# Optimization experiments

Measured on AMD Instinct MI355X. Metric: run time of the kernel, lower is better.

Reference implementation:

```python
import jax, jax.numpy as jnp
import numpy as np
from jax import lax

EMBED = 512
HEADS = 8
KD = EMBED // HEADS  # key_dim == head_dim (value_factor=1)


def setup_inputs() -> dict:
    key = jax.random.key(0)
    ks = jax.random.split(key, 13)
    b, h, w = 4, 128, 128
    s = 0.02
    return {
        "x": jax.random.normal(ks[0], (b, h, w, EMBED), jnp.float32),
        "mask_h": jax.random.normal(ks[1], (HEADS, h, h), jnp.float32),
        "mask_w": jax.random.normal(ks[2], (HEADS, w, w), jnp.float32),
        "Wq": jax.random.normal(ks[3], (EMBED, EMBED), jnp.float32) * s,
        "bq": jnp.zeros((EMBED,), jnp.float32),
        "Wk": jax.random.normal(ks[4], (EMBED, EMBED), jnp.float32) * s,
        "bk": jnp.zeros((EMBED,), jnp.float32),
        "Wv": jax.random.normal(ks[5], (EMBED, EMBED), jnp.float32) * s,
        "bv": jnp.zeros((EMBED,), jnp.float32),
        "lepe_w": jax.random.normal(ks[6], (5, 5, 1, EMBED), jnp.float32) * s,  # depthwise 5x5, HWIO
        "lepe_b": jnp.zeros((EMBED,), jnp.float32),
        "Wo": jax.random.normal(ks[7], (EMBED, EMBED), jnp.float32) * s,
        "bo": jnp.zeros((EMBED,), jnp.float32),
    }


def reference(x, mask_h, mask_w, Wq, bq, Wk, bk, Wv, bv, lepe_w, lepe_b, Wo, bo):
    b, h, w, _ = x.shape
    scaling = KD ** -0.5
    q = x @ Wq + bq                      # (b,h,w,C)
    k = (x @ Wk + bk) * scaling
    v = x @ Wv + bv

    # depthwise-conv positional term (LePE), 5x5 pad 2, groups=C
    lepe = lax.conv_general_dilated(
        v, lepe_w, window_strides=(1, 1), padding=[(2, 2), (2, 2)],
        dimension_numbers=("NHWC", "HWIO", "NHWC"), feature_group_count=EMBED,
    ) + lepe_b

    qr = q.reshape(b, h, w, HEADS, KD)
    kr = k.reshape(b, h, w, HEADS, KD)
    vr = v.reshape(b, h, w, HEADS, KD)

    # width-axis attention (per row), additive per-head decay mask
    sw = jnp.einsum("bhqnd,bhknd->bhnqk", qr, kr) + mask_w[None, None]  # (b,h,n,w,w)
    Aw = jax.nn.softmax(sw, axis=-1)
    o1 = jnp.einsum("bhnqk,bhknd->bhqnd", Aw, vr)                       # (b,h,w,n,d)

    # height-axis attention (per column) on the width-pass output
    sh = jnp.einsum("bqwnd,bkwnd->bwnqk", qr, kr) + mask_h[None, None]  # (b,w,n,h,h)
    Ah = jax.nn.softmax(sh, axis=-1)
    o2 = jnp.einsum("bwnqk,bkwnd->bqwnd", Ah, o1)                       # (b,h,w,n,d)

    out = o2.reshape(b, h, w, EMBED) + lepe
    return out @ Wo + bo
```

## Files before the change

kernel.cpp:

```cpp
#include <hip/hip_runtime.h>
#include <stdint.h>
#include <stddef.h>

typedef unsigned short u16;
typedef __attribute__((ext_vector_type(8))) short bf16x8;
typedef __attribute__((ext_vector_type(4))) short bf16x4;
typedef __attribute__((ext_vector_type(4))) float f32x4;

__device__ __forceinline__ u16 f2bf(float f) {
  union { float f; uint32_t u; } v; v.f = f;
  uint32_t u = v.u;
  return (u16)((u + 0x7FFFu + ((u >> 16) & 1u)) >> 16);
}
__device__ __forceinline__ float bf2f(u16 b) {
  union { uint32_t u; float f; } v; v.u = ((uint32_t)b) << 16;
  return v.f;
}

__device__ __forceinline__ void glds16(const u16* g, u16* l) {
  __builtin_amdgcn_global_load_lds((const __attribute__((address_space(1))) void*)g,
                                   (__attribute__((address_space(3))) void*)l, 16, 0, 0);
}

__device__ __forceinline__ uint32_t lds_addr(const u16* p) {
  return (uint32_t)(uintptr_t)(const __attribute__((address_space(3))) u16*)p;
}

#define MFMA(a, b, c) __builtin_amdgcn_mfma_f32_16x16x32_bf16((a), (b), (c), 0, 0, 0)


__global__ __launch_bounds__(256) void k_cvt_bf16(const float* __restrict__ in,
                                                  u16* __restrict__ out, int n) {
  int i = (blockIdx.x * 256 + threadIdx.x) * 8;
  if (i >= n) return;
  const float4* p = (const float4*)(in + i);
  float4 a = p[0], b = p[1];
  union { bf16x8 v; u16 s[8]; } o;
  o.s[0] = f2bf(a.x); o.s[1] = f2bf(a.y); o.s[2] = f2bf(a.z); o.s[3] = f2bf(a.w);
  o.s[4] = f2bf(b.x); o.s[5] = f2bf(b.y); o.s[6] = f2bf(b.z); o.s[7] = f2bf(b.w);
  *(bf16x8*)(out + i) = o.v;
}


__global__ __launch_bounds__(256) void k_build_w(
    const float* __restrict__ Wq, const float* __restrict__ Wk,
    const float* __restrict__ Wv, const float* __restrict__ Wo,
    const float* __restrict__ bq, const float* __restrict__ bk,
    const float* __restrict__ bv,
    u16* __restrict__ wqkvT, u16* __restrict__ woT, float* __restrict__ bias)
{
  __shared__ u16 tl[64 * 73];
  const int bid = blockIdx.x;
  const int mtx = bid >> 6;
  const int tr = (bid >> 3) & 7, tc = bid & 7;
  const float* W = (mtx == 0) ? Wq : (mtx == 1) ? Wk : (mtx == 2) ? Wv : Wo;
  const float s = (mtx == 1) ? 0.125f : 1.0f;
  const int t = threadIdx.x;
  const int lr = t >> 6, lc = t & 63;
  #pragma unroll
  for (int it = 0; it < 16; ++it) {
    int k = tr * 64 + it * 4 + lr;
    int n = tc * 64 + lc;
    tl[lc * 73 + it * 4 + lr] = f2bf(W[(size_t)k * 512 + n] * s);
  }
  __syncthreads();
  u16* dst = (mtx == 3) ? woT : (wqkvT + (size_t)mtx * 512 * 512);
  #pragma unroll
  for (int it = 0; it < 16; ++it) {
    int n = tc * 64 + it * 4 + lr;
    int k = tr * 64 + lc;
    dst[(size_t)n * 512 + k] = tl[(it * 4 + lr) * 73 + lc];
  }
  if (bid < 6) {
    int i = bid * 256 + t;
    const float* B = (i < 512) ? bq : (i < 1024) ? bk : bv;
    float sc = (i >= 512 && i < 1024) ? 0.125f : 1.0f;
    bias[i] = B[i & 511] * sc;
  }
}


__device__ __forceinline__ void stageH(const u16* __restrict__ src, int ld, size_t grow0,
                                       int kt, int row0, u16* lmat, int t) {
  #pragma unroll
  for (int it = 0; it < 2; ++it) {
    int e = it * 4096 + t * 8;
    int row = row0 + (e >> 6);
    int ch = (e >> 3) & 7;
    int cs = ch ^ (row & 7);
    glds16(src + (grow0 + row) * (size_t)ld + kt * 64 + cs * 8, lmat + row * 64 + ch * 8);
  }
}

__device__ __forceinline__ bf16x8 ldfrag(const u16* lmat, int row, int c) {
  return *(const bf16x8*)(lmat + row * 64 + ((c ^ (row & 7)) << 3));
}

template<bool STAGE, bool VM8>
__device__ __forceinline__ void process_tile(
    const u16* __restrict__ A, int lda, size_t rowA0,
    const u16* __restrict__ BT, int ldb, size_t rowB0,
    u16* LAc, u16* LBc, int nxt,
    int wm, int wn, int fq, int fr, int t,
    f32x4 (&acc)[2][4][2][2])
{
  bf16x8 bA[4][2], bB[2][2][2];
  #pragma unroll
  for (int n = 0; n < 2; ++n)
    #pragma unroll
    for (int kk = 0; kk < 2; ++kk)
      bB[0][n][kk] = ldfrag(LBc, wn * 32 + n * 16 + fr, kk * 4 + fq);
  #pragma unroll
  for (int m = 0; m < 4; ++m)
    #pragma unroll
    for (int kk = 0; kk < 2; ++kk)
      bA[m][kk] = ldfrag(LAc, wm * 64 + m * 16 + fr, kk * 4 + fq);
  __builtin_amdgcn_s_setprio(1);
  #pragma unroll
  for (int m = 0; m < 4; ++m)
    #pragma unroll
    for (int n = 0; n < 2; ++n)
      #pragma unroll
      for (int kk = 0; kk < 2; ++kk)
        acc[0][m][0][n] = MFMA(bA[m][kk], bB[0][n][kk], acc[0][m][0][n]);
  __builtin_amdgcn_s_setprio(0);
  __builtin_amdgcn_s_barrier();
  #pragma unroll
  for (int n = 0; n < 2; ++n)
    #pragma unroll
    for (int kk = 0; kk < 2; ++kk)
      bB[1][n][kk] = ldfrag(LBc, 128 + wn * 32 + n * 16 + fr, kk * 4 + fq);
  if (STAGE) {
    stageH(A, lda, rowA0, nxt, 0, LAc, t);
    stageH(BT, ldb, rowB0, nxt, 0, LBc, t);
  }
  __builtin_amdgcn_s_setprio(1);
  #pragma unroll
  for (int m = 0; m < 4; ++m)
    #pragma unroll
    for (int n = 0; n < 2; ++n)
      #pragma unroll
      for (int kk = 0; kk < 2; ++kk)
        acc[0][m][1][n] = MFMA(bA[m][kk], bB[1][n][kk], acc[0][m][1][n]);
  __builtin_amdgcn_s_setprio(0);
  __builtin_amdgcn_s_barrier();
  #pragma unroll
  for (int m = 0; m < 4; ++m)
    #pragma unroll
    for (int kk = 0; kk < 2; ++kk)
      bA[m][kk] = ldfrag(LAc, 128 + wm * 64 + m * 16 + fr, kk * 4 + fq);
  if (STAGE) stageH(BT, ldb, rowB0, nxt, 128, LBc, t);
  __builtin_amdgcn_s_setprio(1);
  #pragma unroll
  for (int m = 0; m < 4; ++m)
    #pragma unroll
    for (int n = 0; n < 2; ++n)
      #pragma unroll
      for (int kk = 0; kk < 2; ++kk)
        acc[1][m][0][n] = MFMA(bA[m][kk], bB[0][n][kk], acc[1][m][0][n]);
  __builtin_amdgcn_s_setprio(0);
  __builtin_amdgcn_s_barrier();
  if (STAGE) stageH(A, lda, rowA0, nxt, 128, LAc, t);
  __builtin_amdgcn_s_setprio(1);
  #pragma unroll
  for (int m = 0; m < 4; ++m)
    #pragma unroll
    for (int n = 0; n < 2; ++n)
      #pragma unroll
      for (int kk = 0; kk < 2; ++kk)
        acc[1][m][1][n] = MFMA(bA[m][kk], bB[1][n][kk], acc[1][m][1][n]);
  __builtin_amdgcn_s_setprio(0);
  if (VM8) asm volatile("s_waitcnt vmcnt(8)" ::: "memory");
  else     asm volatile("s_waitcnt vmcnt(0)" ::: "memory");
  __builtin_amdgcn_s_barrier();
}

template<bool OUT_F32, int NTN>
__global__ __launch_bounds__(512, 2) void k_gemm256(
    const u16* __restrict__ A, int lda,
    const u16* __restrict__ BT, int ldb,
    const float* __restrict__ bias,
    void* __restrict__ Cp, int ldc)
{
  __shared__ u16 lds[65536];
  u16* LA0 = lds;
  u16* LB0 = lds + 16384;
  u16* LA1 = lds + 32768;
  u16* LB1 = lds + 49152;

  const int t = threadIdx.x, l = t & 63, w = t >> 6;
  const int wm = w >> 2, wn = w & 3;
  const int fq = l >> 4, fr = l & 15;

  const int bid = blockIdx.x;
  const int cpx = gridDim.x >> 3;
  const int swz = (bid & 7) * cpx + (bid >> 3);
  const int tn = swz % NTN, tm = swz / NTN;
  const size_t rowA0 = (size_t)tm * 256;
  const size_t rowB0 = (size_t)tn * 256;

  f32x4 acc[2][4][2][2];
  #pragma unroll
  for (int a = 0; a < 2; ++a)
    #pragma unroll
    for (int m = 0; m < 4; ++m)
      #pragma unroll
      for (int b = 0; b < 2; ++b)
        #pragma unroll
        for (int n = 0; n < 2; ++n) acc[a][m][b][n] = (f32x4){0.f, 0.f, 0.f, 0.f};

  stageH(A,  lda, rowA0, 0, 0,   LA0, t); stageH(A,  lda, rowA0, 0, 128, LA0, t);
  stageH(BT, ldb, rowB0, 0, 0,   LB0, t); stageH(BT, ldb, rowB0, 0, 128, LB0, t);
  stageH(A,  lda, rowA0, 1, 0,   LA1, t); stageH(A,  lda, rowA0, 1, 128, LA1, t);
  stageH(BT, ldb, rowB0, 1, 0,   LB1, t); stageH(BT, ldb, rowB0, 1, 128, LB1, t);
  asm volatile("s_waitcnt vmcnt(8)" ::: "memory");
  __builtin_amdgcn_s_barrier();

  for (int i = 0; i < 3; ++i) {
    process_tile<true, true>(A, lda, rowA0, BT, ldb, rowB0, LA0, LB0, 2 * i + 2,
                             wm, wn, fq, fr, t, acc);
    process_tile<true, true>(A, lda, rowA0, BT, ldb, rowB0, LA1, LB1, 2 * i + 3,
                             wm, wn, fq, fr, t, acc);
  }
  process_tile<false, false>(A, lda, rowA0, BT, ldb, rowB0, LA0, LB0, 0,
                             wm, wn, fq, fr, t, acc);
  process_tile<false, false>(A, lda, rowA0, BT, ldb, rowB0, LA1, LB1, 0,
                             wm, wn, fq, fr, t, acc);

  #pragma unroll
  for (int nh = 0; nh < 2; ++nh)
    #pragma unroll
    for (int n = 0; n < 2; ++n) {
      int col = (int)rowB0 + nh * 128 + wn * 32 + n * 16 + fr;
      float bb = bias[col];
      #pragma unroll
      for (int mh = 0; mh < 2; ++mh)
        #pragma unroll
        for (int m = 0; m < 4; ++m) {
          #pragma unroll
          for (int r = 0; r < 4; ++r) {
            size_t row = rowA0 + mh * 128 + wm * 64 + m * 16 + fq * 4 + r;
            float v = acc[mh][m][nh][n][r] + bb;
            if (OUT_F32) ((float*)Cp)[row * ldc + col] = v;
            else         ((u16*)Cp)[row * ldc + col] = f2bf(v);
          }
        }
    }
}


__global__ __launch_bounds__(256) void k_lepe(
    const u16* __restrict__ qkv, const float* __restrict__ w5,
    const float* __restrict__ lb, u16* __restrict__ outp)
{
  __shared__ u16 wlds[12800];
  #pragma unroll
  for (int j = 0; j < 50; ++j) {
    int idx = j * 256 + threadIdx.x;
    wlds[idx] = f2bf(w5[idx]);
  }
  __syncthreads();

  const int t = threadIdx.x, w = t >> 6, l = t & 63;
  const int c0 = l << 3;
  const int bid = blockIdx.x;
  const int x = (bid & 31) * 4 + w;
  const int y0 = ((bid >> 5) & 15) * 8;
  const int b = bid >> 9;

  float acc[8][8];
  {
    float4 b0 = *(const float4*)(lb + c0);
    float4 b1 = *(const float4*)(lb + c0 + 4);
    #pragma unroll
    for (int tt = 0; tt < 8; ++tt) {
      acc[tt][0] = b0.x; acc[tt][1] = b0.y; acc[tt][2] = b0.z; acc[tt][3] = b0.w;
      acc[tt][4] = b1.x; acc[tt][5] = b1.y; acc[tt][6] = b1.z; acc[tt][7] = b1.w;
    }
  }

  #pragma unroll
  for (int dx = 0; dx < 5; ++dx) {
    int xx = x + dx - 2;
    if ((unsigned)xx < 128u) {
      float wreg[5][8];
      #pragma unroll
      for (int dy = 0; dy < 5; ++dy) {
        union { bf16x8 v; u16 s[8]; } w8;
        w8.v = *(const bf16x8*)(wlds + (dy * 5 + dx) * 512 + c0);
        #pragma unroll
        for (int j = 0; j < 8; ++j) wreg[dy][j] = bf2f(w8.s[j]);
      }
      #pragma unroll
      for (int r = 0; r < 12; ++r) {
        int yy = y0 + r - 2;
        if ((unsigned)yy < 128u) {
          union { bf16x8 v; u16 s[8]; } v8;
          v8.v = *(const bf16x8*)(qkv + (size_t)((b * 128 + yy) * 128 + xx) * 1536
                                  + 1024 + c0);
          float vf[8];
          #pragma unroll
          for (int j = 0; j < 8; ++j) vf[j] = bf2f(v8.s[j]);
          #pragma unroll
          for (int tt = 0; tt < 8; ++tt) {
            int dy = r - tt;
            if (dy >= 0 && dy <= 4) {
              #pragma unroll
              for (int j = 0; j < 8; ++j)
                acc[tt][j] += vf[j] * wreg[dy][j];
            }
          }
        }
      }
    }
  }

  #pragma unroll
  for (int tt = 0; tt < 8; ++tt) {
    size_t tok = (size_t)(b * 128 + y0 + tt) * 128 + x;
    union { bf16x8 v; u16 s[8]; } ov;
    #pragma unroll
    for (int j = 0; j < 8; ++j) ov.s[j] = f2bf(acc[tt][j]);
    *(bf16x8*)(outp + tok * 512 + c0) = ov.v;
  }
}


template<int AXIS>
__global__ __launch_bounds__(512) void k_attn(
    const u16* qkv, const float* __restrict__ mask,
    const u16* __restrict__ lepe, u16* outp)
{
  __shared__ u16 smem[24576];
  u16* q_s = smem;
  u16* k_s = smem + 8192;
  u16* vL  = smem + 16384;
  u16* P   = smem;

  const int t = threadIdx.x, w = t >> 6, l = t & 63;
  const int fq = l >> 4, fr = l & 15;
  const int line = blockIdx.x, head = blockIdx.y, b = blockIdx.z;
  const int coff = head * 64;
  const size_t base0 = (AXIS == 0) ? ((size_t)(b * 128 + line) * 128)
                                   : ((size_t)b * 16384 + line);
  const size_t tstr = (AXIS == 0) ? 1 : 128;

  #pragma unroll
  for (int it = 0; it < 2; ++it) {
    int ee = it * 4096 + t * 8;
    int row = ee >> 6;
    int cs = ((ee >> 3) & 7) ^ (row & 7);
    size_t tok = base0 + (size_t)row * tstr;
    glds16(qkv + tok * 1536 +       coff + cs * 8, q_s + it * 4096 + w * 512);
    glds16(qkv + tok * 1536 + 512 + coff + cs * 8, k_s + it * 4096 + w * 512);
  }
  #pragma unroll
  for (int p = 0; p < 2; ++p) {
    int c = p * 512 + t;
    int kt = (c >> 5) * 4 + ((c >> 1) & 3);
    int d0 = ((c >> 3) & 3) * 16 + (c & 1) * 8;
    size_t tok = base0 + (size_t)kt * tstr;
    glds16(qkv + tok * 1536 + 1024 + coff + d0, vL + c * 8);
  }
  __syncthreads();

  f32x4 acc[8];
  #pragma unroll
  for (int n = 0; n < 8; ++n) acc[n] = (f32x4){0.f, 0.f, 0.f, 0.f};

  #pragma unroll
  for (int kk = 0; kk < 2; ++kk) {
    int arow = w * 16 + fr;
    int ac = (kk * 4 + fq) ^ (arow & 7);
    bf16x8 af = *(const bf16x8*)(q_s + arow * 64 + ac * 8);
    #pragma unroll
    for (int n = 0; n < 8; ++n) {
      int brow = n * 16 + fr;
      int bc = (kk * 4 + fq) ^ (brow & 7);
      bf16x8 bfr = *(const bf16x8*)(k_s + brow * 64 + bc * 8);
      acc[n] = MFMA(af, bfr, acc[n]);
    }
  }

  const float* mbase = mask + (size_t)head * 16384;
  const int q0 = w * 16 + fq * 4;
  #pragma unroll
  for (int n = 0; n < 8; ++n) {
    const float* mp = mbase + (size_t)q0 * 128 + n * 16 + fr;
    #pragma unroll
    for (int r = 0; r < 4; ++r) acc[n][r] += mp[(size_t)r * 128];
  }
  #pragma unroll
  for (int r = 0; r < 4; ++r) {
    float mx = acc[0][r];
    #pragma unroll
    for (int n = 1; n < 8; ++n) mx = fmaxf(mx, acc[n][r]);
    mx = fmaxf(mx, __shfl_xor(mx, 1));
    mx = fmaxf(mx, __shfl_xor(mx, 2));
    mx = fmaxf(mx, __shfl_xor(mx, 4));
    mx = fmaxf(mx, __shfl_xor(mx, 8));
    float sum = 0.f;
    #pragma unroll
    for (int n = 0; n < 8; ++n) {
      float ev = __expf(acc[n][r] - mx);
      acc[n][r] = ev; sum += ev;
    }
    sum += __shfl_xor(sum, 1);
    sum += __shfl_xor(sum, 2);
    sum += __shfl_xor(sum, 4);
    sum += __shfl_xor(sum, 8);
    float inv = 1.0f / sum;
    #pragma unroll
    for (int n = 0; n < 8; ++n) acc[n][r] *= inv;
  }
  __syncthreads();

  #pragma unroll
  for (int r = 0; r < 4; ++r) {
    int row = q0 + r;
    int swz = (row & 7) << 4;
    #pragma unroll
    for (int n = 0; n < 8; ++n) {
      int col = n * 16 + fr;
      *(u16*)((char*)P + row * 256 + ((2 * col) ^ swz)) = f2bf(acc[n][r]);
    }
  }
  __syncthreads();

  f32x4 o[4];
  #pragma unroll
  for (int n = 0; n < 4; ++n) o[n] = (f32x4){0.f, 0.f, 0.f, 0.f};

  const uint32_t vbase = lds_addr(vL) + (uint32_t)(fq * 1024 + fr * 8);
  #pragma unroll
  for (int kt = 0; kt < 4; ++kt) {
    int arow = w * 16 + fr;
    bf16x8 af = *(const bf16x8*)((const char*)P + arow * 256 +
                 (((kt * 4 + fq) << 4) ^ ((arow & 7) << 4)));
    bf16x4 lo0, hi0, lo1, hi1, lo2, hi2, lo3, hi3;
    {
      uint32_t a0 = vbase + kt * 4096;
      uint32_t a1 = a0 + 128;
      uint32_t a2 = a0 + 256;
      uint32_t a3 = a0 + 384;
      asm volatile("ds_read_b64_tr_b16 %0, %1" : "=v"(lo0) : "v"(a0));
      asm volatile("ds_read_b64_tr_b16 %0, %1 offset:512" : "=v"(hi0) : "v"(a0));
      asm volatile("ds_read_b64_tr_b16 %0, %1" : "=v"(lo1) : "v"(a1));
      asm volatile("ds_read_b64_tr_b16 %0, %1 offset:512" : "=v"(hi1) : "v"(a1));
      asm volatile("ds_read_b64_tr_b16 %0, %1" : "=v"(lo2) : "v"(a2));
      asm volatile("ds_read_b64_tr_b16 %0, %1 offset:512" : "=v"(hi2) : "v"(a2));
      asm volatile("ds_read_b64_tr_b16 %0, %1" : "=v"(lo3) : "v"(a3));
      asm volatile("ds_read_b64_tr_b16 %0, %1 offset:512" : "=v"(hi3) : "v"(a3));
    }
    asm volatile("s_waitcnt lgkmcnt(0)" ::: "memory");
    __builtin_amdgcn_sched_barrier(0);
    union { bf16x4 h[2]; bf16x8 v; } u0, u1, u2, u3;
    u0.h[0] = lo0; u0.h[1] = hi0;
    u1.h[0] = lo1; u1.h[1] = hi1;
    u2.h[0] = lo2; u2.h[1] = hi2;
    u3.h[0] = lo3; u3.h[1] = hi3;
    o[0] = MFMA(af, u0.v, o[0]);
    o[1] = MFMA(af, u1.v, o[1]);
    o[2] = MFMA(af, u2.v, o[2]);
    o[3] = MFMA(af, u3.v, o[3]);
  }

  #pragma unroll
  for (int r = 0; r < 4; ++r) {
    int i = q0 + r;
    size_t tok = base0 + (size_t)i * tstr;
    #pragma unroll
    for (int n = 0; n < 4; ++n) {
      int d = n * 16 + fr;
      float v = o[n][r];
      if (AXIS == 1) {
        v += bf2f(lepe[tok * 512 + coff + d]);
        outp[tok * 1536 + coff + d] = f2bf(v);
      } else {
        outp[tok * 1536 + 1024 + coff + d] = f2bf(v);
      }
    }
  }
}


extern "C" void kernel_launch(void* const* d_in, const int* in_sizes, int n_in,
                              void* d_out, int out_size, void* d_ws, size_t ws_size,
                              hipStream_t stream) {
  const float* x  = (const float*)d_in[0];
  const float* mh = (const float*)d_in[1];
  const float* mw = (const float*)d_in[2];
  const float* Wq = (const float*)d_in[3];
  const float* bq = (const float*)d_in[4];
  const float* Wk = (const float*)d_in[5];
  const float* bk = (const float*)d_in[6];
  const float* Wv = (const float*)d_in[7];
  const float* bv = (const float*)d_in[8];
  const float* w5 = (const float*)d_in[9];
  const float* lb = (const float*)d_in[10];
  const float* Wo = (const float*)d_in[11];
  const float* bo = (const float*)d_in[12];

  char* ws = (char*)d_ws;
  u16*   qkv   = (u16*)ws;
  u16*   wqkvT = (u16*)(ws + 201326592);
  u16*   woT   = (u16*)(ws + 202899456);
  float* bqkv  = (float*)(ws + 203423744);

  char* od = (char*)d_out;
  u16* xb   = (u16*)od;
  u16* lepe = (u16*)(od + 67108864);

  k_cvt_bf16<<<16384, 256, 0, stream>>>(x, xb, 33554432);
  k_build_w<<<256, 256, 0, stream>>>(Wq, Wk, Wv, Wo, bq, bk, bv, wqkvT, woT, bqkv);

  k_gemm256<false, 6><<<1536, 512, 0, stream>>>(xb, 512, wqkvT, 512, bqkv,
                                                qkv, 1536);

  k_lepe<<<2048, 256, 0, stream>>>(qkv, w5, lb, lepe);

  k_attn<0><<<dim3(128, 8, 4), 512, 0, stream>>>(qkv, mw, nullptr, qkv);
  k_attn<1><<<dim3(128, 8, 4), 512, 0, stream>>>(qkv, mh, lepe, qkv);

  k_gemm256<true, 2><<<512, 512, 0, stream>>>(qkv, 1536, woT, 512, bo, d_out, 512);
}
```

Before: 416.1 us.

## Fuse fp32-to-bf16 conversion of x into the QKV GEMM A-tile staging

Removes the standalone x conversion kernel and has a new QKV GEMM load fp32 A tiles through registers, converting them to bf16 before writing to LDS. B tiles still use direct global-to-LDS loads. This drops a full write and re-read of the bf16 copy of x (about 64MB of traffic) and one launch. In exchange, each of the six column tiles rereads fp32 A, doubling A read bytes, and the register staging adds VGPR pressure and latency in the pipelined loop.

```diff
diff --git a/kernel.cpp b/kernel.cpp
--- a/kernel.cpp
+++ b/kernel.cpp
@@ -27,19 +27,6 @@
 }
 
 #define MFMA(a, b, c) __builtin_amdgcn_mfma_f32_16x16x32_bf16((a), (b), (c), 0, 0, 0)
-
-
-__global__ __launch_bounds__(256) void k_cvt_bf16(const float* __restrict__ in,
-                                                  u16* __restrict__ out, int n) {
-  int i = (blockIdx.x * 256 + threadIdx.x) * 8;
-  if (i >= n) return;
-  const float4* p = (const float4*)(in + i);
-  float4 a = p[0], b = p[1];
-  union { bf16x8 v; u16 s[8]; } o;
-  o.s[0] = f2bf(a.x); o.s[1] = f2bf(a.y); o.s[2] = f2bf(a.z); o.s[3] = f2bf(a.w);
-  o.s[4] = f2bf(b.x); o.s[5] = f2bf(b.y); o.s[6] = f2bf(b.z); o.s[7] = f2bf(b.w);
-  *(bf16x8*)(out + i) = o.v;
-}
 
 
 __global__ __launch_bounds__(256) void k_build_w(
@@ -96,6 +83,51 @@
   return *(const bf16x8*)(lmat + row * 64 + ((c ^ (row & 7)) << 3));
 }
 
+struct AS { f32x4 v0, v1, v2, v3; };
+
+__device__ __forceinline__ AS stageA_issue(const float* __restrict__ Af, size_t grow0,
+                                           int kt, int row0, int t) {
+  AS s;
+  {
+    int e = t * 8;
+    int row = row0 + (e >> 6);
+    int cs = ((e >> 3) & 7) ^ (row & 7);
+    const float* g = Af + (grow0 + row) * 512 + kt * 64 + cs * 8;
+    s.v0 = *(const f32x4*)g;
+    s.v1 = *(const f32x4*)(g + 4);
+  }
+  {
+    int e = 4096 + t * 8;
+    int row = row0 + (e >> 6);
+    int cs = ((e >> 3) & 7) ^ (row & 7);
+    const float* g = Af + (grow0 + row) * 512 + kt * 64 + cs * 8;
+    s.v2 = *(const f32x4*)g;
+    s.v3 = *(const f32x4*)(g + 4);
+  }
+  return s;
+}
+
+__device__ __forceinline__ void stageA_commit(const AS& s, u16* lmat, int row0, int t) {
+  union { bf16x8 v; u16 e[8]; } o;
+  {
+    int ee = t * 8;
+    int row = row0 + (ee >> 6);
+    int ch = (ee >> 3) & 7;
+    o.e[0] = f2bf(s.v0[0]); o.e[1] = f2bf(s.v0[1]); o.e[2] = f2bf(s.v0[2]); o.e[3] = f2bf(s.v0[3]);
+    o.e[4] = f2bf(s.v1[0]); o.e[5] = f2bf(s.v1[1]); o.e[6] = f2bf(s.v1[2]); o.e[7] = f2bf(s.v1[3]);
+    *(bf16x8*)(lmat + row * 64 + ch * 8) = o.v;
+  }
+  {
+    int ee = 4096 + t * 8;
+    int row = row0 + (ee >> 6);
+    int ch = (ee >> 3) & 7;
+    o.e[0] = f2bf(s.v2[0]); o.e[1] = f2bf(s.v2[1]); o.e[2] = f2bf(s.v2[2]); o.e[3] = f2bf(s.v2[3]);
+    o.e[4] = f2bf(s.v3[0]); o.e[5] = f2bf(s.v3[1]); o.e[6] = f2bf(s.v3[2]); o.e[7] = f2bf(s.v3[3]);
+    *(bf16x8*)(lmat + row * 64 + ch * 8) = o.v;
+  }
+}
+
+
 template<bool STAGE, bool VM8>
 __device__ __forceinline__ void process_tile(
     const u16* __restrict__ A, int lda, size_t rowA0,
@@ -243,6 +275,173 @@
             float v = acc[mh][m][nh][n][r] + bb;
             if (OUT_F32) ((float*)Cp)[row * ldc + col] = v;
             else         ((u16*)Cp)[row * ldc + col] = f2bf(v);
+          }
+        }
+    }
+}
+
+
+template<bool STAGE, int VMN>
+__device__ __forceinline__ void process_tileQKV(
+    const float* __restrict__ Af, size_t rowA0,
+    const u16* __restrict__ BT, size_t rowB0,
+    u16* LAc, u16* LBc, int nxt,
+    int wm, int wn, int fq, int fr, int t,
+    f32x4 (&acc)[2][4][2][2])
+{
+  bf16x8 bA[4][2], bB[2][2][2];
+  AS s0, s1;
+  if (STAGE) s0 = stageA_issue(Af, rowA0, nxt, 0, t);
+  #pragma unroll
+  for (int n = 0; n < 2; ++n)
+    #pragma unroll
+    for (int kk = 0; kk < 2; ++kk)
+      bB[0][n][kk] = ldfrag(LBc, wn * 32 + n * 16 + fr, kk * 4 + fq);
+  #pragma unroll
+  for (int m = 0; m < 4; ++m)
+    #pragma unroll
+    for (int kk = 0; kk < 2; ++kk)
+      bA[m][kk] = ldfrag(LAc, wm * 64 + m * 16 + fr, kk * 4 + fq);
+  __builtin_amdgcn_s_setprio(1);
+  #pragma unroll
+  for (int m = 0; m < 4; ++m)
+    #pragma unroll
+    for (int n = 0; n < 2; ++n)
+      #pragma unroll
+      for (int kk = 0; kk < 2; ++kk)
+        acc[0][m][0][n] = MFMA(bA[m][kk], bB[0][n][kk], acc[0][m][0][n]);
+  __builtin_amdgcn_s_setprio(0);
+  __builtin_amdgcn_s_barrier();
+  #pragma unroll
+  for (int n = 0; n < 2; ++n)
+    #pragma unroll
+    for (int kk = 0; kk < 2; ++kk)
+      bB[1][n][kk] = ldfrag(LBc, 128 + wn * 32 + n * 16 + fr, kk * 4 + fq);
+  if (STAGE) {
+    stageH(BT, 512, rowB0, nxt, 0, LBc, t);
+    s1 = stageA_issue(Af, rowA0, nxt, 128, t);
+    stageA_commit(s0, LAc, 0, t);
+  }
+  __builtin_amdgcn_s_setprio(1);
+  #pragma unroll
+  for (int m = 0; m < 4; ++m)
+    #pragma unroll
+    for (int n = 0; n < 2; ++n)
+      #pragma unroll
+      for (int kk = 0; kk < 2; ++kk)
+        acc[0][m][1][n] = MFMA(bA[m][kk], bB[1][n][kk], acc[0][m][1][n]);
+  __builtin_amdgcn_s_setprio(0);
+  __builtin_amdgcn_s_barrier();
+  #pragma unroll
+  for (int m = 0; m < 4; ++m)
+    #pragma unroll
+    for (int kk = 0; kk < 2; ++kk)
+      bA[m][kk] = ldfrag(LAc, 128 + wm * 64 + m * 16 + fr, kk * 4 + fq);
+  if (STAGE) {
+    stageH(BT, 512, rowB0, nxt, 128, LBc, t);
+    stageA_commit(s1, LAc, 128, t);
+  }
+  __builtin_amdgcn_s_setprio(1);
+  #pragma unroll
+  for (int m = 0; m < 4; ++m)
+    #pragma unroll
+    for (int n = 0; n < 2; ++n)
+      #pragma unroll
+      for (int kk = 0; kk < 2; ++kk)
+        acc[1][m][0][n] = MFMA(bA[m][kk], bB[0][n][kk], acc[1][m][0][n]);
+  __builtin_amdgcn_s_setprio(0);
+  __builtin_amdgcn_s_barrier();
+  __builtin_amdgcn_s_setprio(1);
+  #pragma unroll
+  for (int m = 0; m < 4; ++m)
+    #pragma unroll
+    for (int n = 0; n < 2; ++n)
+      #pragma unroll
+      for (int kk = 0; kk < 2; ++kk)
+        acc[1][m][1][n] = MFMA(bA[m][kk], bB[1][n][kk], acc[1][m][1][n]);
+  __builtin_amdgcn_s_setprio(0);
+  if (VMN == 2) asm volatile("s_waitcnt vmcnt(2)" ::: "memory");
+  else          asm volatile("s_waitcnt vmcnt(0)" ::: "memory");
+  asm volatile("s_waitcnt lgkmcnt(0)" ::: "memory");
+  __builtin_amdgcn_s_barrier();
+}
+
+__global__ __launch_bounds__(512, 2) void k_gemmQKV(
+    const float* __restrict__ Af,
+    const u16* __restrict__ BT,
+    const float* __restrict__ bias,
+    u16* __restrict__ Cp)
+{
+  __shared__ u16 lds[65536];
+  u16* LA0 = lds;
+  u16* LB0 = lds + 16384;
+  u16* LA1 = lds + 32768;
+  u16* LB1 = lds + 49152;
+
+  const int t = threadIdx.x, l = t & 63, w = t >> 6;
+  const int wm = w >> 2, wn = w & 3;
+  const int fq = l >> 4, fr = l & 15;
+
+  const int bid = blockIdx.x;
+  const int cpx = gridDim.x >> 3;
+  const int swz = (bid & 7) * cpx + (bid >> 3);
+  const int tn = swz % 6, tm = swz / 6;
+  const size_t rowA0 = (size_t)tm * 256;
+  const size_t rowB0 = (size_t)tn * 256;
+
+  f32x4 acc[2][4][2][2];
+  #pragma unroll
+  for (int a = 0; a < 2; ++a)
+    #pragma unroll
+    for (int m = 0; m < 4; ++m)
+      #pragma unroll
+      for (int b = 0; b < 2; ++b)
+        #pragma unroll
+        for (int n = 0; n < 2; ++n) acc[a][m][b][n] = (f32x4){0.f, 0.f, 0.f, 0.f};
+
+  {
+    AS p0 = stageA_issue(Af, rowA0, 0, 0, t);
+    AS p1 = stageA_issue(Af, rowA0, 0, 128, t);
+    stageH(BT, 512, rowB0, 0, 0,   LB0, t);
+    stageH(BT, 512, rowB0, 0, 128, LB0, t);
+    stageA_commit(p0, LA0, 0, t);
+    stageA_commit(p1, LA0, 128, t);
+    AS p2 = stageA_issue(Af, rowA0, 1, 0, t);
+    AS p3 = stageA_issue(Af, rowA0, 1, 128, t);
+    stageH(BT, 512, rowB0, 1, 0,   LB1, t);
+    stageH(BT, 512, rowB0, 1, 128, LB1, t);
+    stageA_commit(p2, LA1, 0, t);
+    stageA_commit(p3, LA1, 128, t);
+  }
+  asm volatile("s_waitcnt vmcnt(0)" ::: "memory");
+  asm volatile("s_waitcnt lgkmcnt(0)" ::: "memory");
+  __builtin_amdgcn_s_barrier();
+
+  for (int i = 0; i < 3; ++i) {
+    process_tileQKV<true, 2>(Af, rowA0, BT, rowB0, LA0, LB0, 2 * i + 2,
+                             wm, wn, fq, fr, t, acc);
+    process_tileQKV<true, 2>(Af, rowA0, BT, rowB0, LA1, LB1, 2 * i + 3,
+                             wm, wn, fq, fr, t, acc);
+  }
+  process_tileQKV<false, 0>(Af, rowA0, BT, rowB0, LA0, LB0, 0,
+                            wm, wn, fq, fr, t, acc);
+  process_tileQKV<false, 0>(Af, rowA0, BT, rowB0, LA1, LB1, 0,
+                            wm, wn, fq, fr, t, acc);
+
+  #pragma unroll
+  for (int nh = 0; nh < 2; ++nh)
+    #pragma unroll
+    for (int n = 0; n < 2; ++n) {
+      int col = (int)rowB0 + nh * 128 + wn * 32 + n * 16 + fr;
+      float bb = bias[col];
+      #pragma unroll
+      for (int mh = 0; mh < 2; ++mh)
+        #pragma unroll
+        for (int m = 0; m < 4; ++m) {
+          #pragma unroll
+          for (int r = 0; r < 4; ++r) {
+            size_t row = rowA0 + mh * 128 + wm * 64 + m * 16 + fq * 4 + r;
+            Cp[row * 1536 + col] = f2bf(acc[mh][m][nh][n][r] + bb);
           }
         }
     }
@@ -508,14 +707,11 @@
   float* bqkv  = (float*)(ws + 203423744);
 
   char* od = (char*)d_out;
-  u16* xb   = (u16*)od;
   u16* lepe = (u16*)(od + 67108864);
 
-  k_cvt_bf16<<<16384, 256, 0, stream>>>(x, xb, 33554432);
   k_build_w<<<256, 256, 0, stream>>>(Wq, Wk, Wv, Wo, bq, bk, bv, wqkvT, woT, bqkv);
 
-  k_gemm256<false, 6><<<1536, 512, 0, stream>>>(xb, 512, wqkvT, 512, bqkv,
-                                                qkv, 1536);
+  k_gemmQKV<<<1536, 512, 0, stream>>>(x, wqkvT, bqkv, qkv);
 
   k_lepe<<<2048, 256, 0, stream>>>(qkv, w5, lb, lepe);
 
```

New measurement: 555.8 us. 1.34x slower.
